# Kernel tuning notes

Measured on AMD Instinct MI355X. Metric: run time of the kernel, lower is better.

Reference implementation:

```python
import jax, jax.numpy as jnp
import numpy as np

N = 8192
D = 512
EPS = 1e-12  # F.normalize default eps


def setup_inputs() -> dict:
    key = jax.random.key(0)
    k1, k2 = jax.random.split(key)
    cur = jax.random.normal(k1, (N, D), dtype=jnp.float32)
    # randn -> mixed-sign entries, so every row of (incidence_m > 0) is unique
    # (the only case where the original `incidence_m += head` shapes agree).
    incidence_m = jax.random.normal(k2, (N, N), dtype=jnp.float32)
    return {"cur": cur, "incidence_m": incidence_m}


def reference(cur, incidence_m):
    # construct_directed: dedup rows of (incidence_m > 0); with all rows unique,
    # each node is its own hyperedge leader and head == mask as float, row order
    # preserved. head is built from python ints in torch, hence non-differentiable.
    mask = incidence_m > 0
    head = jax.lax.stop_gradient(mask.astype(incidence_m.dtype))  # [N, N]
    # F.normalize(head, dim=-1): L2 per row with eps clamp
    head = head / jnp.maximum(
        jnp.sqrt(jnp.sum(head * head, axis=-1, keepdims=True)), EPS
    )
    inc = incidence_m + head                          # [N, N]
    edge_fea = inc @ cur                              # [N, D]
    edge_degree = jnp.sum(inc, axis=-1, keepdims=True)  # [N, 1]
    return edge_fea / edge_degree
```

## Files before the change

### kernel.cpp

```cpp
#include <hip/hip_runtime.h>
#include <stdint.h>


#define NROWS 8192
#define DDIM  512

typedef float f32x4 __attribute__((ext_vector_type(4)));
typedef short s16x8 __attribute__((ext_vector_type(8)));

__device__ __forceinline__ unsigned short f2bf(float f) {
  union { float f; unsigned int u; } c; c.f = f;
  unsigned int u = c.u;
  unsigned int r = u + 0x7FFFu + ((u >> 16) & 1u);
  return (unsigned short)(r >> 16);
}

__global__ __launch_bounds__(256) void bprep_kernel(const float* __restrict__ cur,
                                                    unsigned char* __restrict__ bws) {
  int idx = blockIdx.x * 256 + threadIdx.x;
  int n = idx & 511;
  int kg9 = idx >> 9;
  int kt = kg9 >> 3;
  int kg = kg9 & 7;
  int k0 = kt * 64 + kg * 8;
  union { unsigned short h[8]; uint4 q; } u;
#pragma unroll
  for (int e = 0; e < 8; ++e)
    u.h[e] = f2bf(cur[(size_t)(k0 + e) * DDIM + n]);
  int nt = n >> 8, nn = n & 255;
  size_t off = ((size_t)(nt * 128 + kt) << 15) + ((size_t)kg << 12) + ((size_t)nn << 4);
  *(uint4*)(bws + off) = u.q;
}


#define FENCE() __builtin_amdgcn_sched_barrier(0)
#define BARRIER() __builtin_amdgcn_s_barrier()
#define WAITVM1() asm volatile("s_waitcnt vmcnt(1) lgkmcnt(0)" ::: "memory")
#define WAITVM0() asm volatile("s_waitcnt vmcnt(0) lgkmcnt(0)" ::: "memory")

__global__ __launch_bounds__(512, 4) void gemm_kernel(const float* __restrict__ inc,
                                                      const unsigned char* __restrict__ bws,
                                                      float* __restrict__ out) {
  __shared__ __align__(16) unsigned char smem[81920];
  unsigned char* const bBuf0 = smem;
  unsigned char* const bBuf1 = smem + 32768;
  unsigned char* const aBuf0 = smem + 65536;
  unsigned char* const aBuf1 = smem + 69632;
  unsigned char* const mBuf0 = smem + 73728;
  unsigned char* const mBuf1 = smem + 77824;

  const int tid = threadIdx.x;
  const int lane = tid & 63;
  const int wv = tid >> 6;
  const int nt = blockIdx.x;
  const int mt = blockIdx.y;
  const int brow = mt * 32;
  const int bcol = nt * 256;

  const int sm = tid >> 4;
  const int sp = tid & 15;
  const int kgw = sp >> 1, half = sp & 1;
  const float4* gAr = (const float4*)(inc + (size_t)(brow + sm) * NROWS) + sp;
  const int aWr = (kgw << 9) + (((sm ^ kgw)) << 4) + (half << 3);

  const unsigned char* gB = bws + ((size_t)(nt * 128) << 15);
  const int gOffLane = (wv << 10) + (lane << 4);
  const int ldsWave = (wv << 10);

  int aOff[2][2], bOff[2][2];
#pragma unroll
  for (int kh = 0; kh < 2; ++kh) {
    int kg = kh * 4 + (lane >> 4);
#pragma unroll
    for (int g = 0; g < 2; ++g) {
      int r = g * 16 + (lane & 15);
      aOff[kh][g] = (kg << 9) + ((r ^ kg) << 4);
      bOff[kh][g] = (kg << 12) + ((wv * 32 + g * 16 + (lane & 15)) << 4);
    }
  }

  f32x4 acc1[2][2], acc2[2][2];
#pragma unroll
  for (int a = 0; a < 2; ++a)
#pragma unroll
    for (int b = 0; b < 2; ++b) {
      acc1[a][b] = (f32x4){0.f, 0.f, 0.f, 0.f};
      acc2[a][b] = (f32x4){0.f, 0.f, 0.f, 0.f};
    }

  double s1d = 0.0;
  int cnt = 0;
  float4 x, y;

#define ISSUE_A(d, KT) do { d = gAr[(KT) * 16]; } while (0)

#define ISSUE_B(KT, BDST) do {                                                            \
    const unsigned char* _g = gB + ((size_t)(KT) << 15);                                  \
    _Pragma("unroll")                                                                     \
    for (int _s = 0; _s < 4; ++_s)                                                        \
      __builtin_amdgcn_global_load_lds(                                                   \
          (const __attribute__((address_space(1))) unsigned int*)(_g + (_s << 13) + gOffLane), \
          (__attribute__((address_space(3))) unsigned int*)((BDST) + (_s << 13) + ldsWave),    \
          16, 0, 0);                                                                      \
  } while (0)

#define XFORM(s0, ADST, MDST) do {                                                        \
    s1d += (double)s0.x + (double)s0.y + (double)s0.z + (double)s0.w;                     \
    cnt += (s0.x > 0.f) + (s0.y > 0.f) + (s0.z > 0.f) + (s0.w > 0.f);                     \
    unsigned dlo, dhi;                                                                    \
    asm("v_cvt_pk_bf16_f32 %0, %1, %2" : "=v"(dlo) : "v"(s0.x), "v"(s0.y));               \
    asm("v_cvt_pk_bf16_f32 %0, %1, %2" : "=v"(dhi) : "v"(s0.z), "v"(s0.w));               \
    unsigned mlo = (s0.x > 0.f ? 0x3F80u : 0u) | (s0.y > 0.f ? 0x3F800000u : 0u);         \
    unsigned mhi = (s0.z > 0.f ? 0x3F80u : 0u) | (s0.w > 0.f ? 0x3F800000u : 0u);         \
    *(unsigned long long*)((ADST) + aWr) =                                                \
        (unsigned long long)dlo | ((unsigned long long)dhi << 32);                        \
    *(unsigned long long*)((MDST) + aWr) =                                                \
        (unsigned long long)mlo | ((unsigned long long)mhi << 32);                        \
  } while (0)

#define MFMA_TILE(AC, MC, BC) do {                                                        \
    __builtin_amdgcn_s_setprio(1);                                                        \
    _Pragma("unroll")                                                                     \
    for (int kh = 0; kh < 2; ++kh) {                                                      \
      s16x8 af[2], am[2], bfr[2];                                                         \
      _Pragma("unroll")                                                                   \
      for (int g = 0; g < 2; ++g) af[g] = *(const s16x8*)((AC) + aOff[kh][g]);            \
      _Pragma("unroll")                                                                   \
      for (int g = 0; g < 2; ++g) am[g] = *(const s16x8*)((MC) + aOff[kh][g]);            \
      _Pragma("unroll")                                                                   \
      for (int g = 0; g < 2; ++g) bfr[g] = *(const s16x8*)((BC) + bOff[kh][g]);           \
      _Pragma("unroll")                                                                   \
      for (int rg = 0; rg < 2; ++rg)                                                      \
        _Pragma("unroll")                                                                 \
        for (int cg = 0; cg < 2; ++cg) {                                                  \
          acc1[rg][cg] = __builtin_amdgcn_mfma_f32_16x16x32_bf16(af[rg], bfr[cg],         \
                                                                 acc1[rg][cg], 0, 0, 0); \
          acc2[rg][cg] = __builtin_amdgcn_mfma_f32_16x16x32_bf16(am[rg], bfr[cg],         \
                                                                 acc2[rg][cg], 0, 0, 0); \
        }                                                                                 \
    }                                                                                     \
    __builtin_amdgcn_s_setprio(0);                                                        \
  } while (0)

  ISSUE_A(x, 0);
  ISSUE_B(0, bBuf0);
  ISSUE_A(y, 1);
  XFORM(x, aBuf0, mBuf0);
  FENCE();
  WAITVM1();
  FENCE();
  BARRIER();
  FENCE();
  ISSUE_B(1, bBuf1);

  for (int kt = 0; kt < 126; kt += 2) {
    ISSUE_A(x, kt + 2);
    MFMA_TILE(aBuf0, mBuf0, bBuf0);
    XFORM(y, aBuf1, mBuf1);
    FENCE();
    WAITVM1();
    FENCE();
    BARRIER();
    FENCE();
    ISSUE_B(kt + 2, bBuf0);
    ISSUE_A(y, kt + 3);
    MFMA_TILE(aBuf1, mBuf1, bBuf1);
    XFORM(x, aBuf0, mBuf0);
    FENCE();
    WAITVM1();
    FENCE();
    BARRIER();
    FENCE();
    ISSUE_B(kt + 3, bBuf1);
  }

  MFMA_TILE(aBuf0, mBuf0, bBuf0);
  XFORM(y, aBuf1, mBuf1);
  FENCE();
  WAITVM0();
  FENCE();
  BARRIER();
  FENCE();
  MFMA_TILE(aBuf1, mBuf1, bBuf1);

#pragma unroll
  for (int o = 1; o < 16; o <<= 1) {
    s1d += __shfl_xor(s1d, o);
    cnt += __shfl_xor(cnt, o);
  }
  __syncthreads();
  float* const invsS = (float*)bBuf0;
  float* const rdegS = invsS + 32;
  if (sp == 0) {
    double sq = sqrt((double)cnt);
    invsS[sm] = (cnt > 0) ? (float)(1.0 / sq) : 0.0f;
    rdegS[sm] = (float)(1.0 / (s1d + sq));
  }
  __syncthreads();

#pragma unroll
  for (int rg = 0; rg < 2; ++rg) {
    int rb = rg * 16 + ((lane >> 4) << 2);
#pragma unroll
    for (int cg = 0; cg < 2; ++cg) {
      int col = bcol + wv * 32 + cg * 16 + (lane & 15);
#pragma unroll
      for (int r = 0; r < 4; ++r) {
        int rl = rb + r;
        out[(size_t)(brow + rl) * DDIM + col] =
            (acc1[rg][cg][r] + invsS[rl] * acc2[rg][cg][r]) * rdegS[rl];
      }
    }
  }
#undef ISSUE_A
#undef ISSUE_B
#undef XFORM
#undef MFMA_TILE
}

extern "C" void kernel_launch(void* const* d_in, const int* in_sizes, int n_in,
                              void* d_out, int out_size, void* d_ws, size_t ws_size,
                              hipStream_t stream) {
  const float* cur = (const float*)d_in[0];
  const float* incm = (const float*)d_in[1];
  float* out = (float*)d_out;
  unsigned char* bws = (unsigned char*)d_ws;

  hipLaunchKernelGGL(bprep_kernel, dim3((NROWS * DDIM / 8) / 256), dim3(256), 0, stream,
                     cur, bws);
  hipLaunchKernelGGL(gemm_kernel, dim3(2, 256), dim3(512), 0, stream, incm, bws, out);
}
```

Baseline: 182.7 us.

## Load B fragments directly from global into registers, halve block size, swizzle block order

The GEMM no longer stages the bf16 B tile through LDS with global_load_lds. Each wave now loads its B fragments straight from the pre-laid-out workspace into registers, double-buffered across k-steps. Blocks shrink to 4 waves, each covering 64 columns, so LDS drops to about 16 KB and occupancy can rise. Block IDs are remapped so the two column tiles of adjacent row groups run close together and share A rows in cache. The costs are more register pressure from eight B fragments per buffer, and B reads now go through the vector memory path instead of async LDS fills.

```diff
diff --git a/kernel.cpp b/kernel.cpp
--- a/kernel.cpp
+++ b/kernel.cpp
@@ -35,39 +35,35 @@
 
 #define FENCE() __builtin_amdgcn_sched_barrier(0)
 #define BARRIER() __builtin_amdgcn_s_barrier()
-#define WAITVM1() asm volatile("s_waitcnt vmcnt(1) lgkmcnt(0)" ::: "memory")
-#define WAITVM0() asm volatile("s_waitcnt vmcnt(0) lgkmcnt(0)" ::: "memory")
-
-__global__ __launch_bounds__(512, 4) void gemm_kernel(const float* __restrict__ inc,
+#define WAITLGKM() asm volatile("s_waitcnt lgkmcnt(0)" ::: "memory")
+
+__global__ __launch_bounds__(256, 2) void gemm_kernel(const float* __restrict__ inc,
                                                       const unsigned char* __restrict__ bws,
                                                       float* __restrict__ out) {
-  __shared__ __align__(16) unsigned char smem[81920];
-  unsigned char* const bBuf0 = smem;
-  unsigned char* const bBuf1 = smem + 32768;
-  unsigned char* const aBuf0 = smem + 65536;
-  unsigned char* const aBuf1 = smem + 69632;
-  unsigned char* const mBuf0 = smem + 73728;
-  unsigned char* const mBuf1 = smem + 77824;
+  __shared__ __align__(16) unsigned char smem[16640];
+  unsigned char* const aBuf0 = smem;
+  unsigned char* const aBuf1 = smem + 4096;
+  unsigned char* const mBuf0 = smem + 8192;
+  unsigned char* const mBuf1 = smem + 12288;
 
   const int tid = threadIdx.x;
   const int lane = tid & 63;
   const int wv = tid >> 6;
-  const int nt = blockIdx.x;
-  const int mt = blockIdx.y;
+  const int id = blockIdx.x;
+  const int nt = (id >> 2) & 1;
+  const int mt = (id >> 3) * 4 + (id & 3);
   const int brow = mt * 32;
   const int bcol = nt * 256;
 
-  const int sm = tid >> 4;
-  const int sp = tid & 15;
-  const int kgw = sp >> 1, half = sp & 1;
-  const float4* gAr = (const float4*)(inc + (size_t)(brow + sm) * NROWS) + sp;
-  const int aWr = (kgw << 9) + (((sm ^ kgw)) << 4) + (half << 3);
-
-  const unsigned char* gB = bws + ((size_t)(nt * 128) << 15);
-  const int gOffLane = (wv << 10) + (lane << 4);
-  const int ldsWave = (wv << 10);
-
-  int aOff[2][2], bOff[2][2];
+  const int sm = tid >> 3;
+  const int sp = tid & 7;
+  const float4* gAr = (const float4*)(inc + (size_t)(brow + sm) * NROWS) + sp * 2;
+  const int aWr = (sp << 9) + ((sm ^ sp) << 4);
+
+  const unsigned char* gBb = bws + ((size_t)(nt * 128) << 15);
+
+  int aOff[2][2];
+  int bOff[8];
 #pragma unroll
   for (int kh = 0; kh < 2; ++kh) {
     int kg = kh * 4 + (lane >> 4);
@@ -75,121 +71,111 @@
     for (int g = 0; g < 2; ++g) {
       int r = g * 16 + (lane & 15);
       aOff[kh][g] = (kg << 9) + ((r ^ kg) << 4);
-      bOff[kh][g] = (kg << 12) + ((wv * 32 + g * 16 + (lane & 15)) << 4);
     }
-  }
-
-  f32x4 acc1[2][2], acc2[2][2];
+#pragma unroll
+    for (int cg = 0; cg < 4; ++cg)
+      bOff[kh * 4 + cg] = (kg << 12) + ((wv * 64 + cg * 16 + (lane & 15)) << 4);
+  }
+
+  f32x4 acc1[2][4], acc2[2][4];
 #pragma unroll
   for (int a = 0; a < 2; ++a)
 #pragma unroll
-    for (int b = 0; b < 2; ++b) {
+    for (int b = 0; b < 4; ++b) {
       acc1[a][b] = (f32x4){0.f, 0.f, 0.f, 0.f};
       acc2[a][b] = (f32x4){0.f, 0.f, 0.f, 0.f};
     }
 
   double s1d = 0.0;
   int cnt = 0;
-  float4 x, y;
-
-#define ISSUE_A(d, KT) do { d = gAr[(KT) * 16]; } while (0)
-
-#define ISSUE_B(KT, BDST) do {                                                            \
-    const unsigned char* _g = gB + ((size_t)(KT) << 15);                                  \
+  float4 x0, x1, y0, y1;
+  s16x8 bA[8], bB[8];
+
+#define ISSUE_A(d0, d1, KT) do { d0 = gAr[(KT) * 16]; d1 = gAr[(KT) * 16 + 1]; } while (0)
+
+#define LOADB(BS, KT) do {                                                                \
+    const unsigned char* _g = gBb + ((size_t)(KT) << 15);                                 \
     _Pragma("unroll")                                                                     \
-    for (int _s = 0; _s < 4; ++_s)                                                        \
-      __builtin_amdgcn_global_load_lds(                                                   \
-          (const __attribute__((address_space(1))) unsigned int*)(_g + (_s << 13) + gOffLane), \
-          (__attribute__((address_space(3))) unsigned int*)((BDST) + (_s << 13) + ldsWave),    \
-          16, 0, 0);                                                                      \
+    for (int _i = 0; _i < 8; ++_i) BS[_i] = *(const s16x8*)(_g + bOff[_i]);               \
   } while (0)
 
-#define XFORM(s0, ADST, MDST) do {                                                        \
+#define XFORM(s0, s1, ADST, MDST) do {                                                    \
     s1d += (double)s0.x + (double)s0.y + (double)s0.z + (double)s0.w;                     \
+    s1d += (double)s1.x + (double)s1.y + (double)s1.z + (double)s1.w;                     \
     cnt += (s0.x > 0.f) + (s0.y > 0.f) + (s0.z > 0.f) + (s0.w > 0.f);                     \
-    unsigned dlo, dhi;                                                                    \
-    asm("v_cvt_pk_bf16_f32 %0, %1, %2" : "=v"(dlo) : "v"(s0.x), "v"(s0.y));               \
-    asm("v_cvt_pk_bf16_f32 %0, %1, %2" : "=v"(dhi) : "v"(s0.z), "v"(s0.w));               \
-    unsigned mlo = (s0.x > 0.f ? 0x3F80u : 0u) | (s0.y > 0.f ? 0x3F800000u : 0u);         \
-    unsigned mhi = (s0.z > 0.f ? 0x3F80u : 0u) | (s0.w > 0.f ? 0x3F800000u : 0u);         \
-    *(unsigned long long*)((ADST) + aWr) =                                                \
-        (unsigned long long)dlo | ((unsigned long long)dhi << 32);                        \
-    *(unsigned long long*)((MDST) + aWr) =                                                \
-        (unsigned long long)mlo | ((unsigned long long)mhi << 32);                        \
+    cnt += (s1.x > 0.f) + (s1.y > 0.f) + (s1.z > 0.f) + (s1.w > 0.f);                     \
+    uint4 _a, _m;                                                                         \
+    asm("v_cvt_pk_bf16_f32 %0, %1, %2" : "=v"(_a.x) : "v"(s0.x), "v"(s0.y));              \
+    asm("v_cvt_pk_bf16_f32 %0, %1, %2" : "=v"(_a.y) : "v"(s0.z), "v"(s0.w));              \
+    asm("v_cvt_pk_bf16_f32 %0, %1, %2" : "=v"(_a.z) : "v"(s1.x), "v"(s1.y));              \
+    asm("v_cvt_pk_bf16_f32 %0, %1, %2" : "=v"(_a.w) : "v"(s1.z), "v"(s1.w));              \
+    _m.x = (s0.x > 0.f ? 0x3F80u : 0u) | (s0.y > 0.f ? 0x3F800000u : 0u);                 \
+    _m.y = (s0.z > 0.f ? 0x3F80u : 0u) | (s0.w > 0.f ? 0x3F800000u : 0u);                 \
+    _m.z = (s1.x > 0.f ? 0x3F80u : 0u) | (s1.y > 0.f ? 0x3F800000u : 0u);                 \
+    _m.w = (s1.z > 0.f ? 0x3F80u : 0u) | (s1.w > 0.f ? 0x3F800000u : 0u);                 \
+    *(uint4*)((ADST) + aWr) = _a;                                                         \
+    *(uint4*)((MDST) + aWr) = _m;                                                         \
   } while (0)
 
-#define MFMA_TILE(AC, MC, BC) do {                                                        \
+#define MFMA_TILE(AC, MC, BS) do {                                                        \
     __builtin_amdgcn_s_setprio(1);                                                        \
     _Pragma("unroll")                                                                     \
     for (int kh = 0; kh < 2; ++kh) {                                                      \
-      s16x8 af[2], am[2], bfr[2];                                                         \
+      s16x8 af[2], am[2];                                                                 \
       _Pragma("unroll")                                                                   \
       for (int g = 0; g < 2; ++g) af[g] = *(const s16x8*)((AC) + aOff[kh][g]);            \
       _Pragma("unroll")                                                                   \
       for (int g = 0; g < 2; ++g) am[g] = *(const s16x8*)((MC) + aOff[kh][g]);            \
       _Pragma("unroll")                                                                   \
-      for (int g = 0; g < 2; ++g) bfr[g] = *(const s16x8*)((BC) + bOff[kh][g]);           \
-      _Pragma("unroll")                                                                   \
       for (int rg = 0; rg < 2; ++rg)                                                      \
         _Pragma("unroll")                                                                 \
-        for (int cg = 0; cg < 2; ++cg) {                                                  \
-          acc1[rg][cg] = __builtin_amdgcn_mfma_f32_16x16x32_bf16(af[rg], bfr[cg],         \
+        for (int cg = 0; cg < 4; ++cg) {                                                  \
+          acc1[rg][cg] = __builtin_amdgcn_mfma_f32_16x16x32_bf16(af[rg], BS[kh * 4 + cg], \
                                                                  acc1[rg][cg], 0, 0, 0); \
-          acc2[rg][cg] = __builtin_amdgcn_mfma_f32_16x16x32_bf16(am[rg], bfr[cg],         \
+          acc2[rg][cg] = __builtin_amdgcn_mfma_f32_16x16x32_bf16(am[rg], BS[kh * 4 + cg], \
                                                                  acc2[rg][cg], 0, 0, 0); \
         }                                                                                 \
     }                                                                                     \
     __builtin_amdgcn_s_setprio(0);                                                        \
   } while (0)
 
-  ISSUE_A(x, 0);
-  ISSUE_B(0, bBuf0);
-  ISSUE_A(y, 1);
-  XFORM(x, aBuf0, mBuf0);
+#define SYNC() do { FENCE(); WAITLGKM(); FENCE(); BARRIER(); FENCE(); } while (0)
+
+  ISSUE_A(x0, x1, 0);
+  LOADB(bA, 0);
+  ISSUE_A(y0, y1, 1);
+  XFORM(x0, x1, aBuf0, mBuf0);
+  SYNC();
+
+  for (int kt = 0; kt < 126; kt += 2) {
+    ISSUE_A(x0, x1, kt + 2);
+    LOADB(bB, kt + 1);
+    FENCE();
+    MFMA_TILE(aBuf0, mBuf0, bA);
+    XFORM(y0, y1, aBuf1, mBuf1);
+    SYNC();
+    ISSUE_A(y0, y1, kt + 3);
+    LOADB(bA, kt + 2);
+    FENCE();
+    MFMA_TILE(aBuf1, mBuf1, bB);
+    XFORM(x0, x1, aBuf0, mBuf0);
+    SYNC();
+  }
+
+  LOADB(bB, 127);
   FENCE();
-  WAITVM1();
-  FENCE();
-  BARRIER();
-  FENCE();
-  ISSUE_B(1, bBuf1);
-
-  for (int kt = 0; kt < 126; kt += 2) {
-    ISSUE_A(x, kt + 2);
-    MFMA_TILE(aBuf0, mBuf0, bBuf0);
-    XFORM(y, aBuf1, mBuf1);
-    FENCE();
-    WAITVM1();
-    FENCE();
-    BARRIER();
-    FENCE();
-    ISSUE_B(kt + 2, bBuf0);
-    ISSUE_A(y, kt + 3);
-    MFMA_TILE(aBuf1, mBuf1, bBuf1);
-    XFORM(x, aBuf0, mBuf0);
-    FENCE();
-    WAITVM1();
-    FENCE();
-    BARRIER();
-    FENCE();
-    ISSUE_B(kt + 3, bBuf1);
-  }
-
-  MFMA_TILE(aBuf0, mBuf0, bBuf0);
-  XFORM(y, aBuf1, mBuf1);
-  FENCE();
-  WAITVM0();
-  FENCE();
-  BARRIER();
-  FENCE();
-  MFMA_TILE(aBuf1, mBuf1, bBuf1);
-
-#pragma unroll
-  for (int o = 1; o < 16; o <<= 1) {
+  MFMA_TILE(aBuf0, mBuf0, bA);
+  XFORM(y0, y1, aBuf1, mBuf1);
+  SYNC();
+  MFMA_TILE(aBuf1, mBuf1, bB);
+
+#pragma unroll
+  for (int o = 1; o < 8; o <<= 1) {
     s1d += __shfl_xor(s1d, o);
     cnt += __shfl_xor(cnt, o);
   }
   __syncthreads();
-  float* const invsS = (float*)bBuf0;
+  float* const invsS = (float*)aBuf0;
   float* const rdegS = invsS + 32;
   if (sp == 0) {
     double sq = sqrt((double)cnt);
@@ -202,8 +188,8 @@
   for (int rg = 0; rg < 2; ++rg) {
     int rb = rg * 16 + ((lane >> 4) << 2);
 #pragma unroll
-    for (int cg = 0; cg < 2; ++cg) {
-      int col = bcol + wv * 32 + cg * 16 + (lane & 15);
+    for (int cg = 0; cg < 4; ++cg) {
+      int col = bcol + wv * 64 + cg * 16 + (lane & 15);
 #pragma unroll
       for (int r = 0; r < 4; ++r) {
         int rl = rb + r;
@@ -213,9 +199,10 @@
     }
   }
 #undef ISSUE_A
-#undef ISSUE_B
+#undef LOADB
 #undef XFORM
 #undef MFMA_TILE
+#undef SYNC
 }
 
 extern "C" void kernel_launch(void* const* d_in, const int* in_sizes, int n_in,
@@ -228,5 +215,5 @@
 
   hipLaunchKernelGGL(bprep_kernel, dim3((NROWS * DDIM / 8) / 256), dim3(256), 0, stream,
                      cur, bws);
-  hipLaunchKernelGGL(gemm_kernel, dim3(2, 256), dim3(512), 0, stream, incm, bws, out);
-}
+  hipLaunchKernelGGL(gemm_kernel, dim3(512), dim3(256), 0, stream, incm, bws, out);
+}
```

Result: no change. 184.3 us (+0.9%).

## Stage fp32 A tiles via direct-to-LDS loads and read B fragments from global

Applied to the files above, without the earlier changes.

The fp32 incidence tile now goes straight into LDS through global_load_lds with an XOR swizzle. Each wave converts its own A and mask fragments to bf16 at MFMA time instead of writing converted copies to LDS. B fragments are loaded directly from global into registers and double-buffered, which cuts LDS from 80KB to about 16.5KB and removes the separate transform-and-store pass. Row statistics are now computed only by wave 0, and the grid is flattened so the two column tiles of a row block are adjacent. In exchange, every wave repeats the A conversion, and each wave fetches its B fragments from global/L2 instead of sharing them in LDS.

```diff
diff --git a/kernel.cpp b/kernel.cpp
--- a/kernel.cpp
+++ b/kernel.cpp
@@ -35,49 +35,51 @@
 
 #define FENCE() __builtin_amdgcn_sched_barrier(0)
 #define BARRIER() __builtin_amdgcn_s_barrier()
-#define WAITVM1() asm volatile("s_waitcnt vmcnt(1) lgkmcnt(0)" ::: "memory")
-#define WAITVM0() asm volatile("s_waitcnt vmcnt(0) lgkmcnt(0)" ::: "memory")
+#define WAITVM4() asm volatile("s_waitcnt vmcnt(4)" ::: "memory")
+#define MFMA_ __builtin_amdgcn_mfma_f32_16x16x32_bf16
 
 __global__ __launch_bounds__(512, 4) void gemm_kernel(const float* __restrict__ inc,
                                                       const unsigned char* __restrict__ bws,
                                                       float* __restrict__ out) {
-  __shared__ __align__(16) unsigned char smem[81920];
-  unsigned char* const bBuf0 = smem;
-  unsigned char* const bBuf1 = smem + 32768;
-  unsigned char* const aBuf0 = smem + 65536;
-  unsigned char* const aBuf1 = smem + 69632;
-  unsigned char* const mBuf0 = smem + 73728;
-  unsigned char* const mBuf1 = smem + 77824;
+  __shared__ __align__(16) unsigned char smem[16896];
+  unsigned char* const aBuf0 = smem;
+  unsigned char* const aBuf1 = smem + 8192;
+  float* const statS = (float*)(smem + 16384);
 
   const int tid = threadIdx.x;
   const int lane = tid & 63;
   const int wv = tid >> 6;
-  const int nt = blockIdx.x;
-  const int mt = blockIdx.y;
+  const int r = lane & 15;
+  const int q = lane >> 4;
+
+  const int id = blockIdx.x;
+  const int nt = id & 1;
+  const int mt = id >> 1;
   const int brow = mt * 32;
-  const int bcol = nt * 256;
 
   const int sm = tid >> 4;
   const int sp = tid & 15;
-  const int kgw = sp >> 1, half = sp & 1;
-  const float4* gAr = (const float4*)(inc + (size_t)(brow + sm) * NROWS) + sp;
-  const int aWr = (kgw << 9) + (((sm ^ kgw)) << 4) + (half << 3);
+  const int ssp = sp ^ ((sm & 7) << 1);
+  const float* gA = inc + (size_t)(brow + sm) * NROWS + ssp * 4;
+  const int ldsWave = wv << 10;
+
+  int aOff[2][2];
+#pragma unroll
+  for (int kh = 0; kh < 2; ++kh)
+#pragma unroll
+    for (int rg = 0; rg < 2; ++rg) {
+      int row = rg * 16 + r;
+      int s0 = (kh * 8 + q * 2) ^ ((row & 7) << 1);
+      aOff[kh][rg] = row * 256 + (s0 << 4);
+    }
 
   const unsigned char* gB = bws + ((size_t)(nt * 128) << 15);
-  const int gOffLane = (wv << 10) + (lane << 4);
-  const int ldsWave = (wv << 10);
-
-  int aOff[2][2], bOff[2][2];
-#pragma unroll
-  for (int kh = 0; kh < 2; ++kh) {
-    int kg = kh * 4 + (lane >> 4);
-#pragma unroll
-    for (int g = 0; g < 2; ++g) {
-      int r = g * 16 + (lane & 15);
-      aOff[kh][g] = (kg << 9) + ((r ^ kg) << 4);
-      bOff[kh][g] = (kg << 12) + ((wv * 32 + g * 16 + (lane & 15)) << 4);
-    }
-  }
+  int bOff[2][2];
+#pragma unroll
+  for (int kh = 0; kh < 2; ++kh)
+#pragma unroll
+    for (int cg = 0; cg < 2; ++cg)
+      bOff[kh][cg] = ((kh * 4 + q) << 12) + ((wv * 32 + cg * 16 + r) << 4);
 
   f32x4 acc1[2][2], acc2[2][2];
 #pragma unroll
@@ -88,134 +90,147 @@
       acc2[a][b] = (f32x4){0.f, 0.f, 0.f, 0.f};
     }
 
-  double s1d = 0.0;
-  int cnt = 0;
-  float4 x, y;
-
-#define ISSUE_A(d, KT) do { d = gAr[(KT) * 16]; } while (0)
-
-#define ISSUE_B(KT, BDST) do {                                                            \
+  double s1r[2] = {0.0, 0.0};
+  int cnt[2] = {0, 0};
+  const bool statw = (wv == 0);
+
+  s16x8 bX[4], bY[4];
+
+#define ISSUE_A(KT, BUF)                                                                  \
+  __builtin_amdgcn_global_load_lds(                                                       \
+      (const __attribute__((address_space(1))) unsigned int*)(gA + (size_t)(KT) * 64),    \
+      (__attribute__((address_space(3))) unsigned int*)((BUF) + ldsWave), 16, 0, 0)
+
+#define LOADB(BS, KT) do {                                                                \
     const unsigned char* _g = gB + ((size_t)(KT) << 15);                                  \
-    _Pragma("unroll")                                                                     \
-    for (int _s = 0; _s < 4; ++_s)                                                        \
-      __builtin_amdgcn_global_load_lds(                                                   \
-          (const __attribute__((address_space(1))) unsigned int*)(_g + (_s << 13) + gOffLane), \
-          (__attribute__((address_space(3))) unsigned int*)((BDST) + (_s << 13) + ldsWave),    \
-          16, 0, 0);                                                                      \
+    BS[0] = *(const s16x8*)(_g + bOff[0][0]);                                             \
+    BS[1] = *(const s16x8*)(_g + bOff[0][1]);                                             \
+    BS[2] = *(const s16x8*)(_g + bOff[1][0]);                                             \
+    BS[3] = *(const s16x8*)(_g + bOff[1][1]);                                             \
   } while (0)
 
-#define XFORM(s0, ADST, MDST) do {                                                        \
-    s1d += (double)s0.x + (double)s0.y + (double)s0.z + (double)s0.w;                     \
-    cnt += (s0.x > 0.f) + (s0.y > 0.f) + (s0.z > 0.f) + (s0.w > 0.f);                     \
-    unsigned dlo, dhi;                                                                    \
-    asm("v_cvt_pk_bf16_f32 %0, %1, %2" : "=v"(dlo) : "v"(s0.x), "v"(s0.y));               \
-    asm("v_cvt_pk_bf16_f32 %0, %1, %2" : "=v"(dhi) : "v"(s0.z), "v"(s0.w));               \
-    unsigned mlo = (s0.x > 0.f ? 0x3F80u : 0u) | (s0.y > 0.f ? 0x3F800000u : 0u);         \
-    unsigned mhi = (s0.z > 0.f ? 0x3F80u : 0u) | (s0.w > 0.f ? 0x3F800000u : 0u);         \
-    *(unsigned long long*)((ADST) + aWr) =                                                \
-        (unsigned long long)dlo | ((unsigned long long)dhi << 32);                        \
-    *(unsigned long long*)((MDST) + aWr) =                                                \
-        (unsigned long long)mlo | ((unsigned long long)mhi << 32);                        \
+#define MKFRAG(lo, hi, AF, MF) do {                                                       \
+    union { unsigned u[4]; s16x8 s; } _a, _m;                                             \
+    asm("v_cvt_pk_bf16_f32 %0, %1, %2" : "=v"(_a.u[0]) : "v"(lo[0]), "v"(lo[1]));         \
+    asm("v_cvt_pk_bf16_f32 %0, %1, %2" : "=v"(_a.u[1]) : "v"(lo[2]), "v"(lo[3]));         \
+    asm("v_cvt_pk_bf16_f32 %0, %1, %2" : "=v"(_a.u[2]) : "v"(hi[0]), "v"(hi[1]));         \
+    asm("v_cvt_pk_bf16_f32 %0, %1, %2" : "=v"(_a.u[3]) : "v"(hi[2]), "v"(hi[3]));         \
+    _m.u[0] = (lo[0] > 0.f ? 0x3F80u : 0u) | (lo[1] > 0.f ? 0x3F800000u : 0u);            \
+    _m.u[1] = (lo[2] > 0.f ? 0x3F80u : 0u) | (lo[3] > 0.f ? 0x3F800000u : 0u);            \
+    _m.u[2] = (hi[0] > 0.f ? 0x3F80u : 0u) | (hi[1] > 0.f ? 0x3F800000u : 0u);            \
+    _m.u[3] = (hi[2] > 0.f ? 0x3F80u : 0u) | (hi[3] > 0.f ? 0x3F800000u : 0u);            \
+    AF = _a.s; MF = _m.s;                                                                 \
   } while (0)
 
-#define MFMA_TILE(AC, MC, BC) do {                                                        \
+#define KHALF(ABUF, BS, kh) do {                                                          \
+    f32x4 ra0 = *(const f32x4*)((ABUF) + aOff[kh][0]);                                    \
+    f32x4 ra1 = *(const f32x4*)((ABUF) + aOff[kh][0] + 16);                               \
+    f32x4 rb0 = *(const f32x4*)((ABUF) + aOff[kh][1]);                                    \
+    f32x4 rb1 = *(const f32x4*)((ABUF) + aOff[kh][1] + 16);                               \
+    if (statw) {                                                                          \
+      s1r[0] += (double)((ra0[0] + ra0[1]) + (ra0[2] + ra0[3]));                          \
+      s1r[0] += (double)((ra1[0] + ra1[1]) + (ra1[2] + ra1[3]));                          \
+      s1r[1] += (double)((rb0[0] + rb0[1]) + (rb0[2] + rb0[3]));                          \
+      s1r[1] += (double)((rb1[0] + rb1[1]) + (rb1[2] + rb1[3]));                          \
+      cnt[0] += (ra0[0] > 0.f) + (ra0[1] > 0.f) + (ra0[2] > 0.f) + (ra0[3] > 0.f)         \
+              + (ra1[0] > 0.f) + (ra1[1] > 0.f) + (ra1[2] > 0.f) + (ra1[3] > 0.f);        \
+      cnt[1] += (rb0[0] > 0.f) + (rb0[1] > 0.f) + (rb0[2] > 0.f) + (rb0[3] > 0.f)         \
+              + (rb1[0] > 0.f) + (rb1[1] > 0.f) + (rb1[2] > 0.f) + (rb1[3] > 0.f);        \
+    }                                                                                     \
+    s16x8 af0, mf0, af1, mf1;                                                             \
+    MKFRAG(ra0, ra1, af0, mf0);                                                           \
+    MKFRAG(rb0, rb1, af1, mf1);                                                           \
     __builtin_amdgcn_s_setprio(1);                                                        \
-    _Pragma("unroll")                                                                     \
-    for (int kh = 0; kh < 2; ++kh) {                                                      \
-      s16x8 af[2], am[2], bfr[2];                                                         \
-      _Pragma("unroll")                                                                   \
-      for (int g = 0; g < 2; ++g) af[g] = *(const s16x8*)((AC) + aOff[kh][g]);            \
-      _Pragma("unroll")                                                                   \
-      for (int g = 0; g < 2; ++g) am[g] = *(const s16x8*)((MC) + aOff[kh][g]);            \
-      _Pragma("unroll")                                                                   \
-      for (int g = 0; g < 2; ++g) bfr[g] = *(const s16x8*)((BC) + bOff[kh][g]);           \
-      _Pragma("unroll")                                                                   \
-      for (int rg = 0; rg < 2; ++rg)                                                      \
-        _Pragma("unroll")                                                                 \
-        for (int cg = 0; cg < 2; ++cg) {                                                  \
-          acc1[rg][cg] = __builtin_amdgcn_mfma_f32_16x16x32_bf16(af[rg], bfr[cg],         \
-                                                                 acc1[rg][cg], 0, 0, 0); \
-          acc2[rg][cg] = __builtin_amdgcn_mfma_f32_16x16x32_bf16(am[rg], bfr[cg],         \
-                                                                 acc2[rg][cg], 0, 0, 0); \
-        }                                                                                 \
-    }                                                                                     \
+    acc1[0][0] = MFMA_(af0, BS[kh * 2 + 0], acc1[0][0], 0, 0, 0);                         \
+    acc2[0][0] = MFMA_(mf0, BS[kh * 2 + 0], acc2[0][0], 0, 0, 0);                         \
+    acc1[0][1] = MFMA_(af0, BS[kh * 2 + 1], acc1[0][1], 0, 0, 0);                         \
+    acc2[0][1] = MFMA_(mf0, BS[kh * 2 + 1], acc2[0][1], 0, 0, 0);                         \
+    acc1[1][0] = MFMA_(af1, BS[kh * 2 + 0], acc1[1][0], 0, 0, 0);                         \
+    acc2[1][0] = MFMA_(mf1, BS[kh * 2 + 0], acc2[1][0], 0, 0, 0);                         \
+    acc1[1][1] = MFMA_(af1, BS[kh * 2 + 1], acc1[1][1], 0, 0, 0);                         \
+    acc2[1][1] = MFMA_(mf1, BS[kh * 2 + 1], acc2[1][1], 0, 0, 0);                         \
     __builtin_amdgcn_s_setprio(0);                                                        \
   } while (0)
 
-  ISSUE_A(x, 0);
-  ISSUE_B(0, bBuf0);
-  ISSUE_A(y, 1);
-  XFORM(x, aBuf0, mBuf0);
-  FENCE();
-  WAITVM1();
-  FENCE();
+#define TILE(ABUF, BS) do { KHALF(ABUF, BS, 0); KHALF(ABUF, BS, 1); } while (0)
+
+  ISSUE_A(0, aBuf0);
+  FENCE();
+  LOADB(bX, 0);
+  FENCE();
+  WAITVM4();
   BARRIER();
   FENCE();
-  ISSUE_B(1, bBuf1);
 
   for (int kt = 0; kt < 126; kt += 2) {
-    ISSUE_A(x, kt + 2);
-    MFMA_TILE(aBuf0, mBuf0, bBuf0);
-    XFORM(y, aBuf1, mBuf1);
-    FENCE();
-    WAITVM1();
-    FENCE();
+    ISSUE_A(kt + 1, aBuf1);
+    FENCE();
+    LOADB(bY, kt + 1);
+    FENCE();
+    TILE(aBuf0, bX);
+    FENCE();
+    WAITVM4();
     BARRIER();
     FENCE();
-    ISSUE_B(kt + 2, bBuf0);
-    ISSUE_A(y, kt + 3);
-    MFMA_TILE(aBuf1, mBuf1, bBuf1);
-    XFORM(x, aBuf0, mBuf0);
-    FENCE();
-    WAITVM1();
-    FENCE();
+    ISSUE_A(kt + 2, aBuf0);
+    FENCE();
+    LOADB(bX, kt + 2);
+    FENCE();
+    TILE(aBuf1, bY);
+    FENCE();
+    WAITVM4();
     BARRIER();
     FENCE();
-    ISSUE_B(kt + 3, bBuf1);
   }
-
-  MFMA_TILE(aBuf0, mBuf0, bBuf0);
-  XFORM(y, aBuf1, mBuf1);
-  FENCE();
-  WAITVM0();
-  FENCE();
+  ISSUE_A(127, aBuf1);
+  FENCE();
+  LOADB(bY, 127);
+  FENCE();
+  TILE(aBuf0, bX);
+  FENCE();
+  WAITVM4();
   BARRIER();
   FENCE();
-  MFMA_TILE(aBuf1, mBuf1, bBuf1);
-
-#pragma unroll
-  for (int o = 1; o < 16; o <<= 1) {
-    s1d += __shfl_xor(s1d, o);
-    cnt += __shfl_xor(cnt, o);
+  TILE(aBuf1, bY);
+
+  if (statw) {
+#pragma unroll
+    for (int g = 0; g < 2; ++g) {
+      s1r[g] += __shfl_xor(s1r[g], 16);
+      s1r[g] += __shfl_xor(s1r[g], 32);
+      cnt[g] += __shfl_xor(cnt[g], 16);
+      cnt[g] += __shfl_xor(cnt[g], 32);
+    }
+    if (q == 0) {
+      double sq0 = sqrt((double)cnt[0]);
+      double sq1 = sqrt((double)cnt[1]);
+      statS[r]      = (cnt[0] > 0) ? (float)(1.0 / sq0) : 0.0f;
+      statS[16 + r] = (cnt[1] > 0) ? (float)(1.0 / sq1) : 0.0f;
+      statS[32 + r]      = (float)(1.0 / (s1r[0] + sq0));
+      statS[48 + r]      = (float)(1.0 / (s1r[1] + sq1));
+    }
   }
   __syncthreads();
-  float* const invsS = (float*)bBuf0;
-  float* const rdegS = invsS + 32;
-  if (sp == 0) {
-    double sq = sqrt((double)cnt);
-    invsS[sm] = (cnt > 0) ? (float)(1.0 / sq) : 0.0f;
-    rdegS[sm] = (float)(1.0 / (s1d + sq));
-  }
-  __syncthreads();
-
+
+  const float* invsS = statS;
+  const float* rdegS = statS + 32;
 #pragma unroll
   for (int rg = 0; rg < 2; ++rg) {
-    int rb = rg * 16 + ((lane >> 4) << 2);
 #pragma unroll
     for (int cg = 0; cg < 2; ++cg) {
-      int col = bcol + wv * 32 + cg * 16 + (lane & 15);
-#pragma unroll
-      for (int r = 0; r < 4; ++r) {
-        int rl = rb + r;
-        out[(size_t)(brow + rl) * DDIM + col] =
-            (acc1[rg][cg][r] + invsS[rl] * acc2[rg][cg][r]) * rdegS[rl];
+#pragma unroll
+      for (int j = 0; j < 4; ++j) {
+        int row = rg * 16 + q * 4 + j;
+        out[(size_t)(brow + row) * DDIM + nt * 256 + wv * 32 + cg * 16 + r] =
+            (acc1[rg][cg][j] + invsS[row] * acc2[rg][cg][j]) * rdegS[row];
       }
     }
   }
 #undef ISSUE_A
-#undef ISSUE_B
-#undef XFORM
-#undef MFMA_TILE
+#undef LOADB
+#undef MKFRAG
+#undef KHALF
+#undef TILE
 }
 
 extern "C" void kernel_launch(void* const* d_in, const int* in_sizes, int n_in,
@@ -228,5 +243,5 @@
 
   hipLaunchKernelGGL(bprep_kernel, dim3((NROWS * DDIM / 8) / 256), dim3(256), 0, stream,
                      cur, bws);
-  hipLaunchKernelGGL(gemm_kernel, dim3(2, 256), dim3(512), 0, stream, incm, bws, out);
-}
+  hipLaunchKernelGGL(gemm_kernel, dim3(512), dim3(512), 0, stream, incm, bws, out);
+}
```

Measured after the change: 222.1 us. +21.6%, slower.
